# Kernel tuning notes

Measured on AMD Instinct MI355X. Metric: run time of the kernel, lower is better.

Reference implementation:

```python
import jax, jax.numpy as jnp
import numpy as np

E = 16        # n_routed_experts
K = 2         # n_activated_experts (top-k)
DIM = 1024    # model dim
INTER = 704   # moe_inter_dim
B, S = 4, 1024


def setup_inputs() -> dict:
    key = jax.random.key(0)
    ks = jax.random.split(key, 5)
    x = jax.random.normal(ks[0], (B, S, DIM), dtype=jnp.float32)
    Wg = jax.random.normal(ks[1], (E, DIM), dtype=jnp.float32) * 0.02   # gate (Linear, no bias)
    W1 = jax.random.normal(ks[2], (E, DIM, INTER), dtype=jnp.float32) * 0.02
    W3 = jax.random.normal(ks[3], (E, DIM, INTER), dtype=jnp.float32) * 0.02
    W2 = jax.random.normal(ks[4], (E, INTER, DIM), dtype=jnp.float32) * 0.02
    return {"x": x, "Wg": Wg, "W1": W1, "W2": W2, "W3": W3}


def reference(x, Wg, W1, W2, W3):
    # Single-process semantics of MoEWithAll2All: the all2all dispatch/combine is
    # pure communication; the math is: softmax router -> top-k -> renormalize ->
    # per-expert SwiGLU MLP on routed tokens -> weighted combine at original slots.
    Bb, Ss, D = x.shape
    xf = x.reshape(-1, D)                              # [N, D], N = B*S
    logits = xf @ Wg.T                                 # [N, E]
    probs = jax.nn.softmax(logits, axis=-1)
    topw, topi = jax.lax.top_k(probs, K)               # [N, K]
    topw = topw / topw.sum(axis=-1, keepdims=True)
    # gates[n, e] = routed weight of token n for expert e (0 if not routed):
    # identical math to the masked gather/scatter dispatch in the original.
    gates = (jax.nn.one_hot(topi, E, dtype=xf.dtype) * topw[..., None]).sum(axis=1)  # [N, E]
    out = jnp.zeros_like(xf)
    for e in range(E):                                 # small fixed loop over experts
        h = jax.nn.silu(xf @ W1[e]) * (xf @ W3[e])     # SwiGLU expert, [N, INTER]
        out = out + gates[:, e:e + 1] * (h @ W2[e])    # combine with gate weights
    return out.reshape(Bb, Ss, D)
```

## Files before the change

kernel.cpp:

```cpp
#include <hip/hip_runtime.h>

#define NTOK 4096
#define DDIM 1024
#define IDIM 704
#define NEXP 16
#define NSLOT 8192
#define MAXT 128

typedef __attribute__((ext_vector_type(8))) short bf16x8;
typedef __attribute__((ext_vector_type(4))) float f32x4;
typedef __attribute__((ext_vector_type(4))) unsigned short us4;

__device__ __forceinline__ unsigned short f2bf(float f) {
  union { float f; unsigned int u; } v; v.f = f;
  unsigned int r = v.u + 0x7fffu + ((v.u >> 16) & 1u);
  return (unsigned short)(r >> 16);
}

__device__ __forceinline__ void gload_lds16(const void* g, void* l) {
  __builtin_amdgcn_global_load_lds((const __attribute__((address_space(1))) void*)g,
                                   (__attribute__((address_space(3))) void*)l, 16, 0, 0);
}

__global__ void k_convert(const float* __restrict__ x, unsigned short* __restrict__ Xb) {
  int i = blockIdx.x * 256 + threadIdx.x;
  f32x4 v = ((const f32x4*)x)[i];
  us4 o;
#pragma unroll
  for (int j = 0; j < 4; ++j) o[j] = f2bf(v[j]);
  ((us4*)Xb)[i] = o;
}

__global__ void k_router(const float* __restrict__ x, const float* __restrict__ Wg,
                         int* __restrict__ tok_e, float* __restrict__ tok_w) {
  int lane = threadIdx.x & 63;
  int wv = threadIdx.x >> 6;
  int t = blockIdx.x * 4 + wv;
  const f32x4* xr = (const f32x4*)(x + (size_t)t * DDIM);
  f32x4 xv[4];
#pragma unroll
  for (int c = 0; c < 4; ++c) xv[c] = xr[c * 64 + lane];
  float p[NEXP];
#pragma unroll
  for (int e = 0; e < NEXP; ++e) {
    const f32x4* wr = (const f32x4*)(Wg + (size_t)e * DDIM);
    float s = 0.f;
#pragma unroll
    for (int c = 0; c < 4; ++c) {
      f32x4 w4 = wr[c * 64 + lane];
      s += xv[c][0]*w4[0] + xv[c][1]*w4[1] + xv[c][2]*w4[2] + xv[c][3]*w4[3];
    }
    p[e] = s;
  }
#pragma unroll
  for (int off = 32; off >= 1; off >>= 1) {
#pragma unroll
    for (int e = 0; e < NEXP; ++e) p[e] += __shfl_xor(p[e], off);
  }
  int i0 = 0; float b0 = p[0];
#pragma unroll
  for (int e = 1; e < NEXP; ++e) if (p[e] > b0) { b0 = p[e]; i0 = e; }
  int i1 = -1; float b1 = -3.4e38f;
#pragma unroll
  for (int e = 0; e < NEXP; ++e) if (e != i0 && p[e] > b1) { b1 = p[e]; i1 = e; }
  if (lane == 0) {
    float w0 = 1.f / (1.f + __expf(b1 - b0));
    tok_e[2*t] = i0; tok_e[2*t+1] = i1;
    tok_w[2*t] = w0; tok_w[2*t+1] = 1.f - w0;
  }
}

__global__ void k_count_scan(const int* __restrict__ tok_e, int* __restrict__ counts,
                             int* __restrict__ offsets, int* __restrict__ ntiles,
                             int* __restrict__ tile_e, int* __restrict__ tile_m0) {
  __shared__ int h[256 * 17];
  __shared__ int counts_s[NEXP];
  int t = threadIdx.x;
  int c[NEXP];
#pragma unroll
  for (int e = 0; e < NEXP; ++e) c[e] = 0;
  for (int i = t; i < NSLOT; i += 256) {
    int te = tok_e[i];
#pragma unroll
    for (int e = 0; e < NEXP; ++e) c[e] += (te == e) ? 1 : 0;
  }
#pragma unroll
  for (int e = 0; e < NEXP; ++e) h[t * 17 + e] = c[e];
  __syncthreads();
  if (t < NEXP) {
    int s = 0;
    for (int i = 0; i < 256; ++i) s += h[i * 17 + t];
    counts_s[t] = s;
    counts[t] = s;
  }
  __syncthreads();
  if (t == 0) {
    int acc = 0, nt = 0;
    for (int e = 0; e < NEXP; ++e) {
      offsets[e] = acc;
      int cc = counts_s[e];
      for (int m0 = 0; m0 < cc; m0 += 128) { tile_e[nt] = e; tile_m0[nt] = m0; ++nt; }
      acc += cc;
    }
    offsets[NEXP] = acc;
    *ntiles = nt;
  }
}

__global__ void k_scatter2(const int* __restrict__ tok_e, const float* __restrict__ tok_w,
                           const int* __restrict__ offsets, int* __restrict__ token_map,
                           float* __restrict__ gate_w, int* __restrict__ slot_of) {
  int e = blockIdx.x;
  int t = threadIdx.x, lane = t & 63, wv = t >> 6;
  int te[32]; float tw[32];
#pragma unroll
  for (int c = 0; c < 32; ++c) {
    te[c] = tok_e[c * 256 + t];
    tw[c] = tok_w[c * 256 + t];
  }
  __shared__ int wsum[4];
  int run = offsets[e];
  unsigned long long below = (lane == 63) ? 0x7fffffffffffffffull : ((1ull << lane) - 1ull);
#pragma unroll 1
  for (int c = 0; c < 32; ++c) {
    bool f = (te[c] == e);
    unsigned long long m = __ballot(f);
    if (lane == 0) wsum[wv] = __popcll(m);
    __syncthreads();
    int base = run;
    for (int w = 0; w < wv; ++w) base += wsum[w];
    int tot = wsum[0] + wsum[1] + wsum[2] + wsum[3];
    if (f) {
      int i = c * 256 + t;
      int slot = base + __popcll(m & below);
      token_map[slot] = i >> 1;
      gate_w[slot] = tw[c];
      slot_of[i] = slot;
    }
    run += tot;
    __syncthreads();
  }
}

__global__ __launch_bounds__(256, 2)
void k_gemm1(const unsigned short* __restrict__ Xb, const float* __restrict__ W1,
             const float* __restrict__ W3, const int* __restrict__ token_map,
             const float* __restrict__ gate_w, const int* __restrict__ ntiles,
             const int* __restrict__ tile_e, const int* __restrict__ tile_m0,
             const int* __restrict__ offsets, const int* __restrict__ counts,
             unsigned short* __restrict__ H) {
  int ty = blockIdx.y;
  if (ty >= *ntiles) return;
  int e = tile_e[ty], m0 = tile_m0[ty];
  int n0 = blockIdx.x * 128;
  int base_slot = offsets[e] + m0;
  int cnt = counts[e] - m0; if (cnt > 128) cnt = 128;

  __shared__ unsigned short As[128 * 32];
  __shared__ unsigned short B1s[128 * 32];
  __shared__ unsigned short B3s[128 * 32];

  int t = threadIdx.x;
  int src_kg = (t & 3) ^ ((t >> 4) & 3);
  int r0i = base_slot + (t >> 2);        if (r0i > NSLOT - 1) r0i = NSLOT - 1;
  int r1i = base_slot + 64 + (t >> 2);   if (r1i > NSLOT - 1) r1i = NSLOT - 1;
  const unsigned short* ag0 = Xb + (size_t)token_map[r0i] * DDIM + src_kg * 8;
  const unsigned short* ag1 = Xb + (size_t)token_map[r1i] * DDIM + src_kg * 8;
  unsigned short* asd0 = As + t * 8;
  unsigned short* asd1 = As + 2048 + t * 8;

  int nb = t & 31, kb = t >> 5;
  int nloc = nb * 4, kloc = kb * 4;
  int gn = n0 + nloc;
  bool nvalid = gn < IDIM;
  const float* w1p = W1 + (size_t)e * DDIM * IDIM + (size_t)kloc * IDIM + gn;
  const float* w3p = W3 + (size_t)e * DDIM * IDIM + (size_t)kloc * IDIM + gn;
  int wo[4];
#pragma unroll
  for (int j = 0; j < 4; ++j) {
    int row = nloc + j;
    wo[j] = row * 32 + ((((kb >> 1) ^ (row >> 2)) & 3) << 3) + ((kb & 1) << 2);
  }

  int lane = t & 63, wv = t >> 6;
  int wm = (wv >> 1) * 64, wn = (wv & 1) * 64;
  int lm = lane & 15, kg = lane >> 4;
  int ao[4], bo[4];
#pragma unroll
  for (int i = 0; i < 4; ++i) {
    int m = wm + i * 16 + lm;
    ao[i] = m * 32 + (((kg ^ (m >> 2)) & 3) << 3);
    int n = wn + i * 16 + lm;
    bo[i] = n * 32 + (((kg ^ (n >> 2)) & 3) << 3);
  }

  f32x4 acc1[4][4], acc3[4][4];
#pragma unroll
  for (int i = 0; i < 4; ++i)
#pragma unroll
    for (int j = 0; j < 4; ++j) { acc1[i][j] = 0.f; acc3[i][j] = 0.f; }

  for (int k0 = 0; k0 < DDIM; k0 += 32) {
    f32x4 fa[4], fb[4];
#pragma unroll
    for (int j = 0; j < 4; ++j) {
      if (nvalid) {
        fa[j] = *(const f32x4*)(w1p + (size_t)(k0 + j) * IDIM);
        fb[j] = *(const f32x4*)(w3p + (size_t)(k0 + j) * IDIM);
      } else { fa[j] = 0.f; fb[j] = 0.f; }
    }
    __syncthreads();
    gload_lds16(ag0 + k0, asd0);
    gload_lds16(ag1 + k0, asd1);
#pragma unroll
    for (int j = 0; j < 4; ++j) {
      us4 o1, o3;
#pragma unroll
      for (int jj = 0; jj < 4; ++jj) { o1[jj] = f2bf(fa[jj][j]); o3[jj] = f2bf(fb[jj][j]); }
      *(us4*)(B1s + wo[j]) = o1;
      *(us4*)(B3s + wo[j]) = o3;
    }
    __syncthreads();
    bf16x8 av[4], b1v[4], b3v[4];
#pragma unroll
    for (int i = 0; i < 4; ++i) {
      av[i]  = *(const bf16x8*)(As + ao[i]);
      b1v[i] = *(const bf16x8*)(B1s + bo[i]);
      b3v[i] = *(const bf16x8*)(B3s + bo[i]);
    }
#pragma unroll
    for (int mi = 0; mi < 4; ++mi)
#pragma unroll
      for (int ni = 0; ni < 4; ++ni) {
        acc1[mi][ni] = __builtin_amdgcn_mfma_f32_16x16x32_bf16(av[mi], b1v[ni], acc1[mi][ni], 0, 0, 0);
        acc3[mi][ni] = __builtin_amdgcn_mfma_f32_16x16x32_bf16(av[mi], b3v[ni], acc3[mi][ni], 0, 0, 0);
      }
  }

#pragma unroll
  for (int mi = 0; mi < 4; ++mi)
#pragma unroll
    for (int r = 0; r < 4; ++r) {
      int row = wm + mi * 16 + kg * 4 + r;
      if (row < cnt) {
        int slot = base_slot + row;
        float gw = gate_w[slot];
        unsigned short* hrow = H + (size_t)slot * IDIM;
#pragma unroll
        for (int ni = 0; ni < 4; ++ni) {
          int nn = n0 + wn + ni * 16 + lm;
          if (nn < IDIM) {
            float v1 = acc1[mi][ni][r];
            float v3 = acc3[mi][ni][r];
            float h = v1 / (1.f + __expf(-v1)) * v3 * gw;
            hrow[nn] = f2bf(h);
          }
        }
      }
    }
}

__global__ __launch_bounds__(256, 2)
void k_gemm2(const unsigned short* __restrict__ H, const float* __restrict__ W2,
             const int* __restrict__ ntiles, const int* __restrict__ tile_e,
             const int* __restrict__ tile_m0, const int* __restrict__ offsets,
             const int* __restrict__ counts, float* __restrict__ O2) {
  int ty = blockIdx.y;
  if (ty >= *ntiles) return;
  int e = tile_e[ty], m0 = tile_m0[ty];
  int n0 = blockIdx.x * 128;
  int base_slot = offsets[e] + m0;
  int cnt = counts[e] - m0; if (cnt > 128) cnt = 128;

  __shared__ unsigned short As[128 * 32];
  __shared__ unsigned short Bs[128 * 32];

  int t = threadIdx.x;
  int src_kg = (t & 3) ^ ((t >> 4) & 3);
  int r0i = base_slot + (t >> 2);        if (r0i > NSLOT - 1) r0i = NSLOT - 1;
  int r1i = base_slot + 64 + (t >> 2);   if (r1i > NSLOT - 1) r1i = NSLOT - 1;
  const unsigned short* ag0 = H + (size_t)r0i * IDIM + src_kg * 8;
  const unsigned short* ag1 = H + (size_t)r1i * IDIM + src_kg * 8;
  unsigned short* asd0 = As + t * 8;
  unsigned short* asd1 = As + 2048 + t * 8;

  int nb = t & 31, kb = t >> 5;
  int nloc = nb * 4, kloc = kb * 4;
  int gn = n0 + nloc;
  const float* w2p = W2 + (size_t)e * IDIM * DDIM + (size_t)kloc * DDIM + gn;
  int wo[4];
#pragma unroll
  for (int j = 0; j < 4; ++j) {
    int row = nloc + j;
    wo[j] = row * 32 + ((((kb >> 1) ^ (row >> 2)) & 3) << 3) + ((kb & 1) << 2);
  }

  int lane = t & 63, wv = t >> 6;
  int wm = (wv >> 1) * 64, wn = (wv & 1) * 64;
  int lm = lane & 15, kg = lane >> 4;
  int ao[4], bo[4];
#pragma unroll
  for (int i = 0; i < 4; ++i) {
    int m = wm + i * 16 + lm;
    ao[i] = m * 32 + (((kg ^ (m >> 2)) & 3) << 3);
    int n = wn + i * 16 + lm;
    bo[i] = n * 32 + (((kg ^ (n >> 2)) & 3) << 3);
  }

  f32x4 acc[4][4];
#pragma unroll
  for (int i = 0; i < 4; ++i)
#pragma unroll
    for (int j = 0; j < 4; ++j) acc[i][j] = 0.f;

  for (int k0 = 0; k0 < IDIM; k0 += 32) {
    f32x4 fw[4];
#pragma unroll
    for (int j = 0; j < 4; ++j)
      fw[j] = *(const f32x4*)(w2p + (size_t)(k0 + j) * DDIM);
    __syncthreads();
    gload_lds16(ag0 + k0, asd0);
    gload_lds16(ag1 + k0, asd1);
#pragma unroll
    for (int j = 0; j < 4; ++j) {
      us4 o;
#pragma unroll
      for (int jj = 0; jj < 4; ++jj) o[jj] = f2bf(fw[jj][j]);
      *(us4*)(Bs + wo[j]) = o;
    }
    __syncthreads();
    bf16x8 av[4], bv[4];
#pragma unroll
    for (int i = 0; i < 4; ++i) {
      av[i] = *(const bf16x8*)(As + ao[i]);
      bv[i] = *(const bf16x8*)(Bs + bo[i]);
    }
#pragma unroll
    for (int mi = 0; mi < 4; ++mi)
#pragma unroll
      for (int ni = 0; ni < 4; ++ni)
        acc[mi][ni] = __builtin_amdgcn_mfma_f32_16x16x32_bf16(av[mi], bv[ni], acc[mi][ni], 0, 0, 0);
  }

#pragma unroll
  for (int mi = 0; mi < 4; ++mi)
#pragma unroll
    for (int r = 0; r < 4; ++r) {
      int row = wm + mi * 16 + kg * 4 + r;
      if (row < cnt) {
        float* orow = O2 + (size_t)(base_slot + row) * DDIM + n0;
#pragma unroll
        for (int ni = 0; ni < 4; ++ni)
          orow[wn + ni * 16 + lm] = acc[mi][ni][r];
      }
    }
}

__global__ void k_combine(const float* __restrict__ O2, const int* __restrict__ slot_of,
                          float* __restrict__ out) {
  int tk = blockIdx.x, tt = threadIdx.x;
  int s0 = slot_of[2 * tk], s1 = slot_of[2 * tk + 1];
  f32x4 a = ((const f32x4*)(O2 + (size_t)s0 * DDIM))[tt];
  f32x4 b = ((const f32x4*)(O2 + (size_t)s1 * DDIM))[tt];
  ((f32x4*)(out + (size_t)tk * DDIM))[tt] = a + b;
}

extern "C" void kernel_launch(void* const* d_in, const int* in_sizes, int n_in,
                              void* d_out, int out_size, void* d_ws, size_t ws_size,
                              hipStream_t stream) {
  const float* x  = (const float*)d_in[0];
  const float* Wg = (const float*)d_in[1];
  const float* W1 = (const float*)d_in[2];
  const float* W2 = (const float*)d_in[3];
  const float* W3 = (const float*)d_in[4];
  float* out = (float*)d_out;

  char* ws = (char*)d_ws;
  size_t off = 0;
  unsigned short* Xb = (unsigned short*)(ws + off); off += (size_t)NTOK * DDIM * 2;
  unsigned short* H  = (unsigned short*)(ws + off); off += (size_t)NSLOT * IDIM * 2;
  float* O2 = (float*)(ws + off); off += (size_t)NSLOT * DDIM * 4;
  int* counts  = (int*)(ws + off); off += 64;
  int* offsets = (int*)(ws + off); off += 128;
  int* ntiles  = (int*)(ws + off); off += 64;
  int* tile_e  = (int*)(ws + off); off += MAXT * 4;
  int* tile_m0 = (int*)(ws + off); off += MAXT * 4;
  int* tok_e   = (int*)(ws + off); off += NSLOT * 4;
  float* tok_w = (float*)(ws + off); off += NSLOT * 4;
  int* token_map = (int*)(ws + off); off += NSLOT * 4;
  float* gate_w  = (float*)(ws + off); off += NSLOT * 4;
  int* slot_of   = (int*)(ws + off); off += NSLOT * 4;

  k_convert<<<4096, 256, 0, stream>>>(x, Xb);
  k_router<<<1024, 256, 0, stream>>>(x, Wg, tok_e, tok_w);
  k_count_scan<<<1, 256, 0, stream>>>(tok_e, counts, offsets, ntiles, tile_e, tile_m0);
  k_scatter2<<<NEXP, 256, 0, stream>>>(tok_e, tok_w, offsets, token_map, gate_w, slot_of);
  k_gemm1<<<dim3(6, 80), 256, 0, stream>>>(Xb, W1, W3, token_map, gate_w, ntiles, tile_e,
                                           tile_m0, offsets, counts, H);
  k_gemm2<<<dim3(8, 80), 256, 0, stream>>>(H, W2, ntiles, tile_e, tile_m0, offsets, counts, O2);
  k_combine<<<4096, 256, 0, stream>>>(O2, slot_of, out);
}
```

Before: 321.5 us.

## Pre-transpose expert weights to bf16 and load them via direct LDS copies

Adds a per-call transpose kernel that converts W1, W3 and W2 from fp32 [K,N] into bf16 [N,K] buffers, padding W1/W3 to 768 columns. The GEMM kernels then stream weight tiles straight into LDS with global_load_lds, replacing the per-iteration fp32 loads, in-register bf16 conversion and swizzled LDS stores, and they drop the XOR swizzle on the LDS layout. Each weight tile was being re-read and re-converted by every M-tile block, and this removes that repeated fp32 traffic and conversion. The cost is three extra kernels that read all weights once and write bf16 copies, plus possible LDS bank conflicts from the unswizzled layout. gemm2's launch bounds also change to 3 blocks per SM.

```diff
diff --git a/kernel.cpp b/kernel.cpp
--- a/kernel.cpp
+++ b/kernel.cpp
@@ -6,10 +6,12 @@
 #define NEXP 16
 #define NSLOT 8192
 #define MAXT 128
+#define NPAD1 768
 
 typedef __attribute__((ext_vector_type(8))) short bf16x8;
 typedef __attribute__((ext_vector_type(4))) float f32x4;
 typedef __attribute__((ext_vector_type(4))) unsigned short us4;
+typedef __attribute__((ext_vector_type(8))) unsigned short us8;
 
 __device__ __forceinline__ unsigned short f2bf(float f) {
   union { float f; unsigned int u; } v; v.f = f;
@@ -29,6 +31,43 @@
 #pragma unroll
   for (int j = 0; j < 4; ++j) o[j] = f2bf(v[j]);
   ((us4*)Xb)[i] = o;
+}
+
+__global__ void k_wtrans(const float* __restrict__ src, unsigned short* __restrict__ dst,
+                         int ksz, int nsz) {
+  int e = blockIdx.z;
+  int k0 = blockIdx.x * 64, n0 = blockIdx.y * 64;
+  int npad = gridDim.y * 64;
+  src += (size_t)e * ksz * nsz;
+  dst += (size_t)e * npad * ksz;
+  int t = threadIdx.x;
+  int nr = t >> 3, kc0 = (t & 7) * 8;
+  if (n0 >= nsz) {
+    us8 z = (us8)0;
+#pragma unroll
+    for (int p = 0; p < 2; ++p)
+      *(us8*)(dst + (size_t)(n0 + nr + p * 32) * ksz + k0 + kc0) = z;
+    return;
+  }
+  __shared__ unsigned short lds[64 * 76];
+  int nc = (t & 15) * 4, kr = t >> 4;
+#pragma unroll
+  for (int p = 0; p < 4; ++p) {
+    f32x4 v = *(const f32x4*)(src + (size_t)(k0 + kr + p * 16) * nsz + n0 + nc);
+    us4 o;
+#pragma unroll
+    for (int j = 0; j < 4; ++j) o[j] = f2bf(v[j]);
+    *(us4*)(lds + (kr + p * 16) * 76 + nc) = o;
+  }
+  __syncthreads();
+#pragma unroll
+  for (int p = 0; p < 2; ++p) {
+    int row = nr + p * 32;
+    us8 o;
+#pragma unroll
+    for (int j = 0; j < 8; ++j) o[j] = lds[(kc0 + j) * 76 + row];
+    *(us8*)(dst + (size_t)(n0 + row) * ksz + k0 + kc0) = o;
+  }
 }
 
 __global__ void k_router(const float* __restrict__ x, const float* __restrict__ Wg,
@@ -143,8 +182,8 @@
 }
 
 __global__ __launch_bounds__(256, 2)
-void k_gemm1(const unsigned short* __restrict__ Xb, const float* __restrict__ W1,
-             const float* __restrict__ W3, const int* __restrict__ token_map,
+void k_gemm1(const unsigned short* __restrict__ Xb, const unsigned short* __restrict__ W1T,
+             const unsigned short* __restrict__ W3T, const int* __restrict__ token_map,
              const float* __restrict__ gate_w, const int* __restrict__ ntiles,
              const int* __restrict__ tile_e, const int* __restrict__ tile_m0,
              const int* __restrict__ offsets, const int* __restrict__ counts,
@@ -161,26 +200,18 @@
   __shared__ unsigned short B3s[128 * 32];
 
   int t = threadIdx.x;
-  int src_kg = (t & 3) ^ ((t >> 4) & 3);
-  int r0i = base_slot + (t >> 2);        if (r0i > NSLOT - 1) r0i = NSLOT - 1;
-  int r1i = base_slot + 64 + (t >> 2);   if (r1i > NSLOT - 1) r1i = NSLOT - 1;
-  const unsigned short* ag0 = Xb + (size_t)token_map[r0i] * DDIM + src_kg * 8;
-  const unsigned short* ag1 = Xb + (size_t)token_map[r1i] * DDIM + src_kg * 8;
-  unsigned short* asd0 = As + t * 8;
-  unsigned short* asd1 = As + 2048 + t * 8;
-
-  int nb = t & 31, kb = t >> 5;
-  int nloc = nb * 4, kloc = kb * 4;
-  int gn = n0 + nloc;
-  bool nvalid = gn < IDIM;
-  const float* w1p = W1 + (size_t)e * DDIM * IDIM + (size_t)kloc * IDIM + gn;
-  const float* w3p = W3 + (size_t)e * DDIM * IDIM + (size_t)kloc * IDIM + gn;
-  int wo[4];
-#pragma unroll
-  for (int j = 0; j < 4; ++j) {
-    int row = nloc + j;
-    wo[j] = row * 32 + ((((kb >> 1) ^ (row >> 2)) & 3) << 3) + ((kb & 1) << 2);
-  }
+  int row = t >> 2, kc = (t & 3) * 8;
+  int r0i = base_slot + row;      if (r0i > NSLOT - 1) r0i = NSLOT - 1;
+  int r1i = base_slot + 64 + row; if (r1i > NSLOT - 1) r1i = NSLOT - 1;
+  const unsigned short* ag0 = Xb + (size_t)token_map[r0i] * DDIM + kc;
+  const unsigned short* ag1 = Xb + (size_t)token_map[r1i] * DDIM + kc;
+  const unsigned short* b1g0 = W1T + ((size_t)e * NPAD1 + n0 + row) * DDIM + kc;
+  const unsigned short* b1g1 = b1g0 + (size_t)64 * DDIM;
+  const unsigned short* b3g0 = W3T + ((size_t)e * NPAD1 + n0 + row) * DDIM + kc;
+  const unsigned short* b3g1 = b3g0 + (size_t)64 * DDIM;
+  unsigned short* asd0 = As + t * 8;   unsigned short* asd1 = As + 2048 + t * 8;
+  unsigned short* b1d0 = B1s + t * 8;  unsigned short* b1d1 = B1s + 2048 + t * 8;
+  unsigned short* b3d0 = B3s + t * 8;  unsigned short* b3d1 = B3s + 2048 + t * 8;
 
   int lane = t & 63, wv = t >> 6;
   int wm = (wv >> 1) * 64, wn = (wv & 1) * 64;
@@ -188,10 +219,8 @@
   int ao[4], bo[4];
 #pragma unroll
   for (int i = 0; i < 4; ++i) {
-    int m = wm + i * 16 + lm;
-    ao[i] = m * 32 + (((kg ^ (m >> 2)) & 3) << 3);
-    int n = wn + i * 16 + lm;
-    bo[i] = n * 32 + (((kg ^ (n >> 2)) & 3) << 3);
+    ao[i] = (wm + i * 16 + lm) * 32 + kg * 8;
+    bo[i] = (wn + i * 16 + lm) * 32 + kg * 8;
   }
 
   f32x4 acc1[4][4], acc3[4][4];
@@ -201,25 +230,13 @@
     for (int j = 0; j < 4; ++j) { acc1[i][j] = 0.f; acc3[i][j] = 0.f; }
 
   for (int k0 = 0; k0 < DDIM; k0 += 32) {
-    f32x4 fa[4], fb[4];
-#pragma unroll
-    for (int j = 0; j < 4; ++j) {
-      if (nvalid) {
-        fa[j] = *(const f32x4*)(w1p + (size_t)(k0 + j) * IDIM);
-        fb[j] = *(const f32x4*)(w3p + (size_t)(k0 + j) * IDIM);
-      } else { fa[j] = 0.f; fb[j] = 0.f; }
-    }
     __syncthreads();
     gload_lds16(ag0 + k0, asd0);
     gload_lds16(ag1 + k0, asd1);
-#pragma unroll
-    for (int j = 0; j < 4; ++j) {
-      us4 o1, o3;
-#pragma unroll
-      for (int jj = 0; jj < 4; ++jj) { o1[jj] = f2bf(fa[jj][j]); o3[jj] = f2bf(fb[jj][j]); }
-      *(us4*)(B1s + wo[j]) = o1;
-      *(us4*)(B3s + wo[j]) = o3;
-    }
+    gload_lds16(b1g0 + k0, b1d0);
+    gload_lds16(b1g1 + k0, b1d1);
+    gload_lds16(b3g0 + k0, b3d0);
+    gload_lds16(b3g1 + k0, b3d1);
     __syncthreads();
     bf16x8 av[4], b1v[4], b3v[4];
 #pragma unroll
@@ -241,9 +258,9 @@
   for (int mi = 0; mi < 4; ++mi)
 #pragma unroll
     for (int r = 0; r < 4; ++r) {
-      int row = wm + mi * 16 + kg * 4 + r;
-      if (row < cnt) {
-        int slot = base_slot + row;
+      int orow = wm + mi * 16 + kg * 4 + r;
+      if (orow < cnt) {
+        int slot = base_slot + orow;
         float gw = gate_w[slot];
         unsigned short* hrow = H + (size_t)slot * IDIM;
 #pragma unroll
@@ -260,8 +277,8 @@
     }
 }
 
-__global__ __launch_bounds__(256, 2)
-void k_gemm2(const unsigned short* __restrict__ H, const float* __restrict__ W2,
+__global__ __launch_bounds__(256, 3)
+void k_gemm2(const unsigned short* __restrict__ H, const unsigned short* __restrict__ W2T,
              const int* __restrict__ ntiles, const int* __restrict__ tile_e,
              const int* __restrict__ tile_m0, const int* __restrict__ offsets,
              const int* __restrict__ counts, float* __restrict__ O2) {
@@ -276,24 +293,15 @@
   __shared__ unsigned short Bs[128 * 32];
 
   int t = threadIdx.x;
-  int src_kg = (t & 3) ^ ((t >> 4) & 3);
-  int r0i = base_slot + (t >> 2);        if (r0i > NSLOT - 1) r0i = NSLOT - 1;
-  int r1i = base_slot + 64 + (t >> 2);   if (r1i > NSLOT - 1) r1i = NSLOT - 1;
-  const unsigned short* ag0 = H + (size_t)r0i * IDIM + src_kg * 8;
-  const unsigned short* ag1 = H + (size_t)r1i * IDIM + src_kg * 8;
-  unsigned short* asd0 = As + t * 8;
-  unsigned short* asd1 = As + 2048 + t * 8;
-
-  int nb = t & 31, kb = t >> 5;
-  int nloc = nb * 4, kloc = kb * 4;
-  int gn = n0 + nloc;
-  const float* w2p = W2 + (size_t)e * IDIM * DDIM + (size_t)kloc * DDIM + gn;
-  int wo[4];
-#pragma unroll
-  for (int j = 0; j < 4; ++j) {
-    int row = nloc + j;
-    wo[j] = row * 32 + ((((kb >> 1) ^ (row >> 2)) & 3) << 3) + ((kb & 1) << 2);
-  }
+  int row = t >> 2, kc = (t & 3) * 8;
+  int r0i = base_slot + row;      if (r0i > NSLOT - 1) r0i = NSLOT - 1;
+  int r1i = base_slot + 64 + row; if (r1i > NSLOT - 1) r1i = NSLOT - 1;
+  const unsigned short* ag0 = H + (size_t)r0i * IDIM + kc;
+  const unsigned short* ag1 = H + (size_t)r1i * IDIM + kc;
+  const unsigned short* bg0 = W2T + ((size_t)e * DDIM + n0 + row) * IDIM + kc;
+  const unsigned short* bg1 = bg0 + (size_t)64 * IDIM;
+  unsigned short* asd0 = As + t * 8;  unsigned short* asd1 = As + 2048 + t * 8;
+  unsigned short* bd0 = Bs + t * 8;   unsigned short* bd1 = Bs + 2048 + t * 8;
 
   int lane = t & 63, wv = t >> 6;
   int wm = (wv >> 1) * 64, wn = (wv & 1) * 64;
@@ -301,10 +309,8 @@
   int ao[4], bo[4];
 #pragma unroll
   for (int i = 0; i < 4; ++i) {
-    int m = wm + i * 16 + lm;
-    ao[i] = m * 32 + (((kg ^ (m >> 2)) & 3) << 3);
-    int n = wn + i * 16 + lm;
-    bo[i] = n * 32 + (((kg ^ (n >> 2)) & 3) << 3);
+    ao[i] = (wm + i * 16 + lm) * 32 + kg * 8;
+    bo[i] = (wn + i * 16 + lm) * 32 + kg * 8;
   }
 
   f32x4 acc[4][4];
@@ -314,20 +320,11 @@
     for (int j = 0; j < 4; ++j) acc[i][j] = 0.f;
 
   for (int k0 = 0; k0 < IDIM; k0 += 32) {
-    f32x4 fw[4];
-#pragma unroll
-    for (int j = 0; j < 4; ++j)
-      fw[j] = *(const f32x4*)(w2p + (size_t)(k0 + j) * DDIM);
     __syncthreads();
     gload_lds16(ag0 + k0, asd0);
     gload_lds16(ag1 + k0, asd1);
-#pragma unroll
-    for (int j = 0; j < 4; ++j) {
-      us4 o;
-#pragma unroll
-      for (int jj = 0; jj < 4; ++jj) o[jj] = f2bf(fw[jj][j]);
-      *(us4*)(Bs + wo[j]) = o;
-    }
+    gload_lds16(bg0 + k0, bd0);
+    gload_lds16(bg1 + k0, bd1);
     __syncthreads();
     bf16x8 av[4], bv[4];
 #pragma unroll
@@ -346,12 +343,12 @@
   for (int mi = 0; mi < 4; ++mi)
 #pragma unroll
     for (int r = 0; r < 4; ++r) {
-      int row = wm + mi * 16 + kg * 4 + r;
-      if (row < cnt) {
-        float* orow = O2 + (size_t)(base_slot + row) * DDIM + n0;
+      int orow = wm + mi * 16 + kg * 4 + r;
+      if (orow < cnt) {
+        float* op = O2 + (size_t)(base_slot + orow) * DDIM + n0;
 #pragma unroll
         for (int ni = 0; ni < 4; ++ni)
-          orow[wn + ni * 16 + lm] = acc[mi][ni][r];
+          op[wn + ni * 16 + lm] = acc[mi][ni][r];
       }
     }
 }
@@ -380,6 +377,9 @@
   unsigned short* Xb = (unsigned short*)(ws + off); off += (size_t)NTOK * DDIM * 2;
   unsigned short* H  = (unsigned short*)(ws + off); off += (size_t)NSLOT * IDIM * 2;
   float* O2 = (float*)(ws + off); off += (size_t)NSLOT * DDIM * 4;
+  unsigned short* W1T = (unsigned short*)(ws + off); off += (size_t)NEXP * NPAD1 * DDIM * 2;
+  unsigned short* W3T = (unsigned short*)(ws + off); off += (size_t)NEXP * NPAD1 * DDIM * 2;
+  unsigned short* W2T = (unsigned short*)(ws + off); off += (size_t)NEXP * DDIM * IDIM * 2;
   int* counts  = (int*)(ws + off); off += 64;
   int* offsets = (int*)(ws + off); off += 128;
   int* ntiles  = (int*)(ws + off); off += 64;
@@ -395,8 +395,11 @@
   k_router<<<1024, 256, 0, stream>>>(x, Wg, tok_e, tok_w);
   k_count_scan<<<1, 256, 0, stream>>>(tok_e, counts, offsets, ntiles, tile_e, tile_m0);
   k_scatter2<<<NEXP, 256, 0, stream>>>(tok_e, tok_w, offsets, token_map, gate_w, slot_of);
-  k_gemm1<<<dim3(6, 80), 256, 0, stream>>>(Xb, W1, W3, token_map, gate_w, ntiles, tile_e,
+  k_wtrans<<<dim3(16, 12, NEXP), 256, 0, stream>>>(W1, W1T, DDIM, IDIM);
+  k_wtrans<<<dim3(16, 12, NEXP), 256, 0, stream>>>(W3, W3T, DDIM, IDIM);
+  k_wtrans<<<dim3(11, 16, NEXP), 256, 0, stream>>>(W2, W2T, IDIM, DDIM);
+  k_gemm1<<<dim3(6, 80), 256, 0, stream>>>(Xb, W1T, W3T, token_map, gate_w, ntiles, tile_e,
                                            tile_m0, offsets, counts, H);
-  k_gemm2<<<dim3(8, 80), 256, 0, stream>>>(H, W2, ntiles, tile_e, tile_m0, offsets, counts, O2);
+  k_gemm2<<<dim3(8, 80), 256, 0, stream>>>(H, W2T, ntiles, tile_e, tile_m0, offsets, counts, O2);
   k_combine<<<4096, 256, 0, stream>>>(O2, slot_of, out);
 }
```

Measured after the change: 317.7 us. About the same (-1.2%).
